# Kernel optimization log

Hardware: AMD Instinct MI355X
Metric: run time of the kernel (lower is better)

Reference implementation:

```python
import jax, jax.numpy as jnp
import numpy as np

EMBED_DIM = 512
NUM_HEADS = 8
HEAD_DIM = EMBED_DIM // NUM_HEADS
N_NODES = 65536
EPS = 1e-5


def setup_inputs() -> dict:
    key = jax.random.key(0)
    ks = jax.random.split(key, 16)
    std = 0.02
    E, F = EMBED_DIM, 4 * EMBED_DIM
    return {
        "x": jax.random.normal(ks[0], (N_NODES, E), jnp.float32),
        "Wq": jax.random.normal(ks[1], (E, E), jnp.float32) * std,
        "bq": jnp.zeros((E,), jnp.float32),
        "Wk": jax.random.normal(ks[2], (E, E), jnp.float32) * std,
        "bk": jnp.zeros((E,), jnp.float32),
        "Wv": jax.random.normal(ks[3], (E, E), jnp.float32) * std,
        "bv": jnp.zeros((E,), jnp.float32),
        "Wo": jax.random.normal(ks[4], (E, E), jnp.float32) * std,
        "bo": jnp.zeros((E,), jnp.float32),
        "W1": jax.random.normal(ks[5], (F, E), jnp.float32) * std,
        "b1": jnp.zeros((F,), jnp.float32),
        "W2": jax.random.normal(ks[6], (E, F), jnp.float32) * std,
        "b2": jnp.zeros((E,), jnp.float32),
        "g1": jnp.ones((E,), jnp.float32),
        "beta1": jnp.zeros((E,), jnp.float32),
        "g2": jnp.ones((E,), jnp.float32),
        "beta2": jnp.zeros((E,), jnp.float32),
    }


def _layernorm(x, g, b):
    mu = jnp.mean(x, axis=-1, keepdims=True)
    var = jnp.mean(jnp.square(x - mu), axis=-1, keepdims=True)
    return (x - mu) * jax.lax.rsqrt(var + EPS) * g + b


def reference(x, Wq, bq, Wk, bk, Wv, bv, Wo, bo, W1, b1, W2, b2, g1, beta1, g2, beta2):
    N = x.shape[0]
    H, D = NUM_HEADS, HEAD_DIM
    residual = x
    h = _layernorm(x, g1, beta1)
    q = (h @ Wq.T + bq).reshape(N, H, D)
    k = (h @ Wk.T + bk).reshape(N, H, D)
    v = (h @ Wv.T + bv).reshape(N, H, D)
    # per-node attention across heads: scores (N, H, H)
    scores = jnp.einsum('nhd,ngd->nhg', q, k) / np.float32(np.sqrt(D))
    attn = jax.nn.softmax(scores, axis=-1)
    out = jnp.einsum('nhg,ngd->nhd', attn, v).reshape(N, H * D)
    out = out @ Wo.T + bo
    x = residual + out  # dropout is identity in eval
    residual = x
    h = _layernorm(x, g2, beta2)
    ff = jax.nn.relu(h @ W1.T + b1) @ W2.T + b2
    return residual + ff
```

## Files before the change

kernel.cpp:

```cpp
#include <hip/hip_runtime.h>
#include <hip/hip_bf16.h>
#include <stdint.h>

typedef __hip_bfloat16 bf16;
typedef short bf16x8 __attribute__((ext_vector_type(8)));
typedef float f32x4 __attribute__((ext_vector_type(4)));

typedef __attribute__((address_space(1))) const unsigned int as1_uint;
typedef __attribute__((address_space(3))) unsigned int as3_uint;

__device__ __forceinline__ void async_copy16(const void* g, void* l) {
    __builtin_amdgcn_global_load_lds((as1_uint*)g, (as3_uint*)l, 16, 0, 0);
}

__device__ __forceinline__ float b2f(unsigned short u) {
    union { unsigned int i; float f; } c; c.i = ((unsigned int)u) << 16; return c.f;
}
__device__ __forceinline__ unsigned short f2b(float f) {
    union { float f; unsigned int i; } c; c.f = f;
    unsigned int i = c.i;
    i += 0x7fffu + ((i >> 16) & 1u);
    return (unsigned short)(i >> 16);
}

__global__ __launch_bounds__(256)
void cvt_kernel(const float* __restrict__ in, bf16* __restrict__ out)
{
    const int i = (blockIdx.x * 256 + threadIdx.x) * 8;
    const float4 a = *(const float4*)(in + i);
    const float4 b = *(const float4*)(in + i + 4);
    union { uint4 v; unsigned short s[8]; } u;
    u.s[0] = f2b(a.x); u.s[1] = f2b(a.y); u.s[2] = f2b(a.z); u.s[3] = f2b(a.w);
    u.s[4] = f2b(b.x); u.s[5] = f2b(b.y); u.s[6] = f2b(b.z); u.s[7] = f2b(b.w);
    *(uint4*)((unsigned short*)out + i) = u.v;
}

__global__ __launch_bounds__(256)
void ln_kernel(const float* __restrict__ x, const float* __restrict__ g,
               const float* __restrict__ beta, bf16* __restrict__ out)
{
    const int w = threadIdx.x >> 6, l = threadIdx.x & 63;
    const int n = blockIdx.x * 4 + w;

    const float* xr = x + (size_t)n * 512 + l * 8;
    const float4 a = *(const float4*)xr;
    const float4 b = *(const float4*)(xr + 4);
    float f[8] = {a.x, a.y, a.z, a.w, b.x, b.y, b.z, b.w};

    float s = 0.f, q = 0.f;
#pragma unroll
    for (int i = 0; i < 8; ++i) { s += f[i]; q += f[i] * f[i]; }
#pragma unroll
    for (int o = 32; o > 0; o >>= 1) { s += __shfl_xor(s, o); q += __shfl_xor(q, o); }
    const float mean = s * (1.f / 512.f);
    const float var  = q * (1.f / 512.f) - mean * mean;
    const float rstd = rsqrtf(var + 1e-5f);

    const float4 g0 = *(const float4*)(g + l * 8);
    const float4 g1 = *(const float4*)(g + l * 8 + 4);
    const float4 b0 = *(const float4*)(beta + l * 8);
    const float4 b1 = *(const float4*)(beta + l * 8 + 4);
    const float gg[8] = {g0.x,g0.y,g0.z,g0.w,g1.x,g1.y,g1.z,g1.w};
    const float bb[8] = {b0.x,b0.y,b0.z,b0.w,b1.x,b1.y,b1.z,b1.w};

    union { uint4 v; unsigned short s[8]; } o;
#pragma unroll
    for (int i = 0; i < 8; ++i)
        o.s[i] = f2b((f[i] - mean) * rstd * gg[i] + bb[i]);
    *(uint4*)((unsigned short*)out + (size_t)n * 512 + l * 8) = o.v;
}

__global__ __launch_bounds__(256)
void attn_kernel(const bf16* __restrict__ qkv, bf16* __restrict__ out)
{
    __shared__ unsigned short sm[4][1536];
    const int w = threadIdx.x >> 6, l = threadIdx.x & 63;
    const int n = blockIdx.x * 4 + w;

    const uint4* src = (const uint4*)((const unsigned short*)qkv + (size_t)n * 1536);
    uint4* dst = (uint4*)sm[w];
#pragma unroll
    for (int i = 0; i < 3; ++i) dst[i * 64 + l] = src[i * 64 + l];
    __syncthreads();

    const int h = l >> 3, gi = l & 7;
    const unsigned short* qrow = sm[w] + h * 64;
    const unsigned short* krow = sm[w] + 512 + gi * 64;
    float s = 0.f;
#pragma unroll
    for (int jj = 0; jj < 8; ++jj) {
        union { uint4 v; unsigned short s8[8]; } qa, ka;
        qa.v = *(const uint4*)(qrow + jj * 8);
        ka.v = *(const uint4*)(krow + jj * 8);
#pragma unroll
        for (int j = 0; j < 8; ++j) s += b2f(qa.s8[j]) * b2f(ka.s8[j]);
    }
    s *= 0.125f;

    float m = s;
#pragma unroll
    for (int o = 1; o < 8; o <<= 1) m = fmaxf(m, __shfl_xor(m, o));
    float e = __expf(s - m);
    float d = e;
#pragma unroll
    for (int o = 1; o < 8; o <<= 1) d += __shfl_xor(d, o);
    const float p = e / d;

    float acc[8];
#pragma unroll
    for (int j = 0; j < 8; ++j) acc[j] = 0.f;
    const int j8 = (l & 7) * 8;
#pragma unroll
    for (int gg = 0; gg < 8; ++gg) {
        const float pg = __shfl(p, (l & 56) | gg);
        union { uint4 v; unsigned short s8[8]; } va;
        va.v = *(const uint4*)(sm[w] + 1024 + gg * 64 + j8);
#pragma unroll
        for (int j = 0; j < 8; ++j) acc[j] += pg * b2f(va.s8[j]);
    }
    union { uint4 v; unsigned short s8[8]; } o;
#pragma unroll
    for (int j = 0; j < 8; ++j) o.s8[j] = f2b(acc[j]);
    *(uint4*)((unsigned short*)out + (size_t)n * 512 + h * 64 + j8) = o.v;
}

#define EPI_PLAIN 0
#define EPI_RES   1
#define EPI_RELU  2

template<int MODE>
__global__ __launch_bounds__(512, 2)
void gemm_bt(const bf16* __restrict__ A,
             const bf16* __restrict__ B0, const bf16* __restrict__ B1,
             const bf16* __restrict__ B2,
             const float* __restrict__ bias0, const float* __restrict__ bias1,
             const float* __restrict__ bias2,
             const float* __restrict__ res,
             void* __restrict__ C,
             int K, int Nper, int ldc)
{
    __shared__ bf16 As[2][2][8192];
    __shared__ bf16 Bs[2][2][8192];

    const int tid = threadIdx.x;
    const int w = tid >> 6, l = tid & 63;

    const int nbx = gridDim.x;
    const int nwg = nbx * (int)gridDim.y;
    int lid = blockIdx.y * nbx + blockIdx.x;
    {
        const int q = nwg >> 3, r = nwg & 7;
        const int xcd = lid & 7, idx = lid >> 3;
        lid = (xcd < r ? xcd * (q + 1) : r * (q + 1) + (xcd - r) * q) + idx;
    }
    const int bx = lid % nbx, by = lid / nbx;

    const int rowBase = by * 256;
    const int colBase = bx * 256;
    const int sel = colBase / Nper;
    const bf16*  B    = (sel == 0) ? B0 : (sel == 1) ? B1 : B2;
    const float* bias = (sel == 0) ? bias0 : (sel == 1) ? bias1 : bias2;
    const int colInB = colBase - sel * Nper;

    const bf16* Ag = A + (size_t)rowBase * K;
    const bf16* Bg = B + (size_t)colInB * K;

    const int wr = w >> 2, wc = w & 3;
    const int ml = l & 15;
    const int kc = l >> 4;
    const int rdoff = ((kc ^ ((ml >> 1) & 3)) << 3);

    const int s_row = l >> 2;
    const int s_koff = (((l & 3) ^ ((l >> 3) & 3)) << 3);

    auto stA = [&](int t, int half) {
#pragma unroll
        for (int c = 0; c < 2; ++c) {
            const int q = (w << 1) | c;
            const int p = q >> 3, rr = q & 7;
            const bf16* src = Ag + (size_t)(half * 128 + rr * 16 + s_row) * K
                            + (t << 6) + p * 32 + s_koff;
            async_copy16(src, &As[t & 1][half][q << 9]);
        }
    };
    auto stB = [&](int t, int half) {
#pragma unroll
        for (int c = 0; c < 2; ++c) {
            const int q = (w << 1) | c;
            const int p = q >> 3, rr = q & 7;
            const bf16* src = Bg + (size_t)(half * 128 + rr * 16 + s_row) * K
                            + (t << 6) + p * 32 + s_koff;
            async_copy16(src, &Bs[t & 1][half][q << 9]);
        }
    };

    const int bRow = ((wc & 1) << 6) + ml;
    const int bHalf = wc >> 1;

    f32x4 acc[8][4];
#pragma unroll
    for (int i = 0; i < 8; ++i)
#pragma unroll
        for (int j = 0; j < 4; ++j) acc[i][j] = (f32x4)(0.f);

    bf16x8 af[4][2], bf[4][2];

#define LDA(SLOT, MI, KS) \
    (*(const bf16x8*)(&As[SLOT][wr][(KS) * 4096 + ((MI) * 16 + ml) * 32 + rdoff]))
#define LDB(SLOT, NI, KS) \
    (*(const bf16x8*)(&Bs[SLOT][bHalf][(KS) * 4096 + (bRow + (NI) * 16) * 32 + rdoff]))

#define MMQ(MG, NG) \
    do { \
        _Pragma("unroll") \
        for (int mi = 0; mi < 4; ++mi) \
        _Pragma("unroll") \
        for (int nj = 0; nj < 2; ++nj) \
        _Pragma("unroll") \
        for (int ks = 0; ks < 2; ++ks) \
            acc[(MG)*4+mi][(NG)*2+nj] = __builtin_amdgcn_mfma_f32_16x16x32_bf16( \
                af[mi][ks], bf[(NG)*2+nj][ks], acc[(MG)*4+mi][(NG)*2+nj], 0, 0, 0); \
    } while (0)

#define SYNC_IN()  do { __builtin_amdgcn_s_barrier(); \
                        __builtin_amdgcn_sched_barrier(0); \
                        asm volatile("s_waitcnt lgkmcnt(0)" ::: "memory"); \
                        __builtin_amdgcn_sched_barrier(0); } while (0)
#define SYNC_OUT() do { __builtin_amdgcn_s_barrier(); \
                        __builtin_amdgcn_sched_barrier(0); } while (0)

    const int NT = K >> 6;
    const int NI = NT >> 1;

    stA(0, 0); stA(0, 1); stB(0, 0); stB(0, 1);
    stA(1, 0); stB(1, 0);
    asm volatile("s_waitcnt vmcnt(4)" ::: "memory");
    __builtin_amdgcn_s_barrier();
    __builtin_amdgcn_sched_barrier(0);

    for (int i = 0; i < NI; ++i) {
        const int t1 = 2 * i + 1;
        const bool pf = (t1 + 1 < NT);

#pragma unroll
        for (int mi = 0; mi < 4; ++mi) { af[mi][0] = LDA(0, mi, 0); af[mi][1] = LDA(0, mi, 1); }
#pragma unroll
        for (int nj = 0; nj < 2; ++nj) { bf[nj][0] = LDB(0, nj, 0); bf[nj][1] = LDB(0, nj, 1); }
        stA(t1, 1);
        SYNC_IN();
        __builtin_amdgcn_s_setprio(1); MMQ(0, 0); __builtin_amdgcn_s_setprio(0);
        SYNC_OUT();

#pragma unroll
        for (int nj = 2; nj < 4; ++nj) { bf[nj][0] = LDB(0, nj, 0); bf[nj][1] = LDB(0, nj, 1); }
        stB(t1, 1);
        SYNC_IN();
        __builtin_amdgcn_s_setprio(1); MMQ(0, 1); __builtin_amdgcn_s_setprio(0);
        SYNC_OUT();

#pragma unroll
        for (int mi = 0; mi < 4; ++mi) { af[mi][0] = LDA(0, mi + 4, 0); af[mi][1] = LDA(0, mi + 4, 1); }
        if (pf) stB(t1 + 1, 0);
        SYNC_IN();
        __builtin_amdgcn_s_setprio(1); MMQ(1, 0); __builtin_amdgcn_s_setprio(0);
        SYNC_OUT();

        if (pf) stB(t1 + 1, 1);
        __builtin_amdgcn_s_barrier();
        __builtin_amdgcn_sched_barrier(0);
        __builtin_amdgcn_s_setprio(1); MMQ(1, 1); __builtin_amdgcn_s_setprio(0);
        if (pf) asm volatile("s_waitcnt vmcnt(4)" ::: "memory");
        else    asm volatile("s_waitcnt vmcnt(0)" ::: "memory");
        SYNC_OUT();

#pragma unroll
        for (int mi = 0; mi < 4; ++mi) { af[mi][0] = LDA(1, mi, 0); af[mi][1] = LDA(1, mi, 1); }
#pragma unroll
        for (int nj = 0; nj < 2; ++nj) { bf[nj][0] = LDB(1, nj, 0); bf[nj][1] = LDB(1, nj, 1); }
        if (pf) stA(t1 + 1, 0);
        SYNC_IN();
        __builtin_amdgcn_s_setprio(1); MMQ(0, 0); __builtin_amdgcn_s_setprio(0);
        SYNC_OUT();

#pragma unroll
        for (int nj = 2; nj < 4; ++nj) { bf[nj][0] = LDB(1, nj, 0); bf[nj][1] = LDB(1, nj, 1); }
        if (pf) stA(t1 + 1, 1);
        SYNC_IN();
        __builtin_amdgcn_s_setprio(1); MMQ(0, 1); __builtin_amdgcn_s_setprio(0);
        SYNC_OUT();

#pragma unroll
        for (int mi = 0; mi < 4; ++mi) { af[mi][0] = LDA(1, mi + 4, 0); af[mi][1] = LDA(1, mi + 4, 1); }
        if (pf) stB(t1 + 2, 0);
        SYNC_IN();
        __builtin_amdgcn_s_setprio(1); MMQ(1, 0); __builtin_amdgcn_s_setprio(0);
        SYNC_OUT();

        if (pf) stA(t1 + 2, 0);
        __builtin_amdgcn_s_barrier();
        __builtin_amdgcn_sched_barrier(0);
        __builtin_amdgcn_s_setprio(1); MMQ(1, 1); __builtin_amdgcn_s_setprio(0);
        if (pf) asm volatile("s_waitcnt vmcnt(4)" ::: "memory");
        if (i < NI - 1) SYNC_OUT();
    }

    float bv[4];
#pragma unroll
    for (int ni = 0; ni < 4; ++ni)
        bv[ni] = bias[colInB + (wc << 6) + (ni << 4) + ml];

#pragma unroll
    for (int mi = 0; mi < 8; ++mi) {
#pragma unroll
        for (int r4 = 0; r4 < 4; ++r4) {
            const int row = rowBase + (wr << 7) + (mi << 4) + (kc << 2) + r4;
            const size_t rowoff = (size_t)row * ldc;
#pragma unroll
            for (int ni = 0; ni < 4; ++ni) {
                const int gcol = colBase + (wc << 6) + (ni << 4) + ml;
                float v = acc[mi][ni][r4] + bv[ni];
                if (MODE == EPI_RELU) v = fmaxf(v, 0.f);
                if (MODE == EPI_RES) {
                    v += res[rowoff + gcol];
                    ((float*)C)[rowoff + gcol] = v;
                } else {
                    ((unsigned short*)C)[rowoff + gcol] = f2b(v);
                }
            }
        }
    }
#undef LDA
#undef LDB
#undef MMQ
#undef SYNC_IN
#undef SYNC_OUT
}

extern "C" void kernel_launch(void* const* d_in, const int* in_sizes, int n_in,
                              void* d_out, int out_size, void* d_ws, size_t ws_size,
                              hipStream_t stream)
{
    const float* x   = (const float*)d_in[0];
    const float* Wq  = (const float*)d_in[1];
    const float* bq  = (const float*)d_in[2];
    const float* Wk  = (const float*)d_in[3];
    const float* bk  = (const float*)d_in[4];
    const float* Wv  = (const float*)d_in[5];
    const float* bv  = (const float*)d_in[6];
    const float* Wo  = (const float*)d_in[7];
    const float* bo  = (const float*)d_in[8];
    const float* W1  = (const float*)d_in[9];
    const float* b1  = (const float*)d_in[10];
    const float* W2  = (const float*)d_in[11];
    const float* b2  = (const float*)d_in[12];
    const float* g1  = (const float*)d_in[13];
    const float* be1 = (const float*)d_in[14];
    const float* g2  = (const float*)d_in[15];
    const float* be2 = (const float*)d_in[16];

    const int N = 65536;

    bf16* Wqb = (bf16*)d_ws;
    bf16* Wkb = Wqb + 262144;
    bf16* Wvb = Wkb + 262144;
    bf16* Wob = Wvb + 262144;
    bf16* W1b = Wob + 262144;
    bf16* W2b = W1b + 1048576;
    const size_t wts_bytes = 6ull * 1024 * 1024;
    bf16* t64 = (bf16*)((char*)d_ws + wts_bytes);
    const size_t t64_bytes = (size_t)N * 512 * 2;
    bf16* cb  = (bf16*)((char*)d_ws + wts_bytes + t64_bytes);
    const size_t used = wts_bytes + t64_bytes;
    const size_t avail = ws_size > used ? ws_size - used : 0;
    int Nc = 32768;
    while (Nc > 256 && (size_t)Nc * 4096 > avail) Nc >>= 1;

    float* x2 = (float*)d_out;
    dim3 blk(256);
    dim3 blk5(512);

    cvt_kernel<<<262144 / 2048, blk, 0, stream>>>(Wq, Wqb);
    cvt_kernel<<<262144 / 2048, blk, 0, stream>>>(Wk, Wkb);
    cvt_kernel<<<262144 / 2048, blk, 0, stream>>>(Wv, Wvb);
    cvt_kernel<<<262144 / 2048, blk, 0, stream>>>(Wo, Wob);
    cvt_kernel<<<1048576 / 2048, blk, 0, stream>>>(W1, W1b);
    cvt_kernel<<<1048576 / 2048, blk, 0, stream>>>(W2, W2b);

    ln_kernel<<<N / 4, blk, 0, stream>>>(x, g1, be1, t64);

    for (int r0 = 0; r0 < N; r0 += Nc) {
        gemm_bt<EPI_PLAIN><<<dim3(6, Nc / 256), blk5, 0, stream>>>(
            t64 + (size_t)r0 * 512, Wqb, Wkb, Wvb, bq, bk, bv, nullptr,
            cb, 512, 512, 1536);
        attn_kernel<<<Nc / 4, blk, 0, stream>>>(cb, t64 + (size_t)r0 * 512);
    }

    gemm_bt<EPI_RES><<<dim3(2, N / 256), blk5, 0, stream>>>(
        t64, Wob, Wob, Wob, bo, bo, bo, x, x2, 512, 512, 512);

    ln_kernel<<<N / 4, blk, 0, stream>>>(x2, g2, be2, t64);

    for (int r0 = 0; r0 < N; r0 += Nc) {
        gemm_bt<EPI_RELU><<<dim3(8, Nc / 256), blk5, 0, stream>>>(
            t64 + (size_t)r0 * 512, W1b, W1b, W1b, b1, b1, b1, nullptr,
            cb, 512, 2048, 2048);
        gemm_bt<EPI_RES><<<dim3(2, Nc / 256), blk5, 0, stream>>>(
            cb, W2b, W2b, W2b, b2, b2, b2, x2 + (size_t)r0 * 512,
            x2 + (size_t)r0 * 512, 2048, 512, 512);
    }
}
```

Before: 925.5 us.

## Fuse FFN up-projection, ReLU, and down-projection into one kernel

Replaces the two chunked FFN GEMMs with a single kernel that keeps a 64-node tile of the normalized activations in LDS. It computes 256-wide slices of the hidden layer with ReLU into double-buffered LDS and accumulates the W2 product in registers, so the large bf16 hidden tensor never goes to global memory. Weights are read straight from global memory with no LDS staging, and each block handles only 64 nodes with a single block per CU, which may cost weight bandwidth and latency hiding. The load order in the existing GEMM prologue is also interleaved, and the chunk-size workspace check is adjusted.

New measurement: 1.128 ms. +21.9%, slower.

```diff
diff --git a/kernel.cpp b/kernel.cpp
--- a/kernel.cpp
+++ b/kernel.cpp
@@ -232,7 +232,7 @@
     const int NT = K >> 6;
     const int NI = NT >> 1;
 
-    stA(0, 0); stA(0, 1); stB(0, 0); stB(0, 1);
+    stA(0, 0); stB(0, 0); stA(0, 1); stB(0, 1);
     stA(1, 0); stB(1, 0);
     asm volatile("s_waitcnt vmcnt(4)" ::: "memory");
     __builtin_amdgcn_s_barrier();
@@ -334,6 +334,139 @@
 #undef MMQ
 #undef SYNC_IN
 #undef SYNC_OUT
+}
+
+__global__ __launch_bounds__(512, 1)
+void ffn_fused(const bf16* __restrict__ h2,
+               const bf16* __restrict__ W1,
+               const bf16* __restrict__ W2,
+               const float* __restrict__ b1,
+               const float* __restrict__ b2,
+               float* __restrict__ xio)
+{
+    __shared__ bf16 hs[16 * 64 * 32];
+    __shared__ bf16 ps[2 * 64 * 256];
+
+    const int tid = threadIdx.x;
+    const int w = tid >> 6, l = tid & 63;
+    const int node0 = blockIdx.x * 64;
+    const int ml = l & 15, lh = l >> 4;
+
+    {
+        const int sr = l >> 2;
+        const int sk = (((l & 3) ^ ((sr >> 1) & 3)) << 3);
+#pragma unroll
+        for (int j = 0; j < 8; ++j) {
+            const int q = j * 8 + w;
+            const int pl = q >> 2, rg = q & 3;
+            const bf16* src = h2 + (size_t)(node0 + rg * 16 + sr) * 512
+                            + pl * 32 + sk;
+            async_copy16(src, &hs[q << 9]);
+        }
+    }
+    asm volatile("s_waitcnt vmcnt(0)" ::: "memory");
+    __syncthreads();
+
+    const int rdk = ((lh ^ ((ml >> 1) & 3)) << 3);
+
+    f32x4 acc2[4][4];
+#pragma unroll
+    for (int i = 0; i < 4; ++i)
+#pragma unroll
+        for (int j = 0; j < 4; ++j) acc2[i][j] = (f32x4)(0.f);
+
+    for (int s = 0; s < 8; ++s) {
+        f32x4 pacc[2][4];
+#pragma unroll
+        for (int i = 0; i < 2; ++i)
+#pragma unroll
+            for (int j = 0; j < 4; ++j) pacc[i][j] = (f32x4)(0.f);
+
+        const bf16* w1base = W1 + (size_t)(s * 256 + w * 32) * 512;
+#pragma unroll
+        for (int kt = 0; kt < 8; ++kt) {
+            bf16x8 afp[2][2], bfp[4][2];
+#pragma unroll
+            for (int mi = 0; mi < 2; ++mi)
+#pragma unroll
+                for (int ks = 0; ks < 2; ++ks)
+                    afp[mi][ks] = *(const bf16x8*)(w1base
+                        + (size_t)(mi * 16 + ml) * 512 + kt * 64 + ks * 32 + lh * 8);
+#pragma unroll
+            for (int ni = 0; ni < 4; ++ni)
+#pragma unroll
+                for (int ks = 0; ks < 2; ++ks)
+                    bfp[ni][ks] = *(const bf16x8*)(&hs[(kt * 2 + ks) * 2048
+                        + (ni * 16 + ml) * 32 + rdk]);
+#pragma unroll
+            for (int mi = 0; mi < 2; ++mi)
+#pragma unroll
+                for (int ni = 0; ni < 4; ++ni)
+#pragma unroll
+                    for (int ks = 0; ks < 2; ++ks)
+                        pacc[mi][ni] = __builtin_amdgcn_mfma_f32_16x16x32_bf16(
+                            afp[mi][ks], bfp[ni][ks], pacc[mi][ni], 0, 0, 0);
+        }
+
+        const int buf = (s & 1) << 14;
+#pragma unroll
+        for (int mi = 0; mi < 2; ++mi) {
+            const float4 bb = *(const float4*)(b1 + s * 256 + w * 32 + mi * 16 + lh * 4);
+            const float b4[4] = {bb.x, bb.y, bb.z, bb.w};
+#pragma unroll
+            for (int ni = 0; ni < 4; ++ni) {
+                const int row = ni * 16 + ml;
+                const int col = (w * 32 + mi * 16 + lh * 4) ^ ((row & 7) << 3);
+                union { uint2 v; unsigned short s4[4]; } o;
+#pragma unroll
+                for (int r = 0; r < 4; ++r)
+                    o.s4[r] = f2b(fmaxf(pacc[mi][ni][r] + b4[r], 0.f));
+                *(uint2*)(&ps[buf + row * 256 + col]) = o.v;
+            }
+        }
+        __syncthreads();
+
+        const bf16* w2base = W2 + (size_t)(w * 64) * 2048 + s * 256;
+#pragma unroll
+        for (int kt2 = 0; kt2 < 8; ++kt2) {
+            bf16x8 af2[4], bf2[4];
+#pragma unroll
+            for (int of = 0; of < 4; ++of)
+                af2[of] = *(const bf16x8*)(w2base
+                    + (size_t)(of * 16 + ml) * 2048 + kt2 * 32 + lh * 8);
+#pragma unroll
+            for (int nf = 0; nf < 4; ++nf) {
+                const int row = nf * 16 + ml;
+                const int col = (kt2 * 32 + lh * 8) ^ ((row & 7) << 3);
+                bf2[nf] = *(const bf16x8*)(&ps[buf + row * 256 + col]);
+            }
+#pragma unroll
+            for (int of = 0; of < 4; ++of)
+#pragma unroll
+                for (int nf = 0; nf < 4; ++nf)
+                    acc2[of][nf] = __builtin_amdgcn_mfma_f32_16x16x32_bf16(
+                        af2[of], bf2[nf], acc2[of][nf], 0, 0, 0);
+        }
+        __syncthreads();
+    }
+
+#pragma unroll
+    for (int of = 0; of < 4; ++of) {
+        const int oc0 = w * 64 + of * 16 + lh * 4;
+        const float4 bb = *(const float4*)(b2 + oc0);
+#pragma unroll
+        for (int nf = 0; nf < 4; ++nf) {
+            const int node = node0 + nf * 16 + ml;
+            float4* p = (float4*)(xio + (size_t)node * 512 + oc0);
+            const float4 r = *p;
+            float4 o;
+            o.x = acc2[of][nf][0] + r.x + bb.x;
+            o.y = acc2[of][nf][1] + r.y + bb.y;
+            o.z = acc2[of][nf][2] + r.z + bb.z;
+            o.w = acc2[of][nf][3] + r.w + bb.w;
+            *p = o;
+        }
+    }
 }
 
 extern "C" void kernel_launch(void* const* d_in, const int* in_sizes, int n_in,
@@ -373,7 +506,7 @@
     const size_t used = wts_bytes + t64_bytes;
     const size_t avail = ws_size > used ? ws_size - used : 0;
     int Nc = 32768;
-    while (Nc > 256 && (size_t)Nc * 4096 > avail) Nc >>= 1;
+    while (Nc > 256 && (size_t)Nc * 3072 > avail) Nc >>= 1;
 
     float* x2 = (float*)d_out;
     dim3 blk(256);
@@ -400,12 +533,5 @@
 
     ln_kernel<<<N / 4, blk, 0, stream>>>(x2, g2, be2, t64);
 
-    for (int r0 = 0; r0 < N; r0 += Nc) {
-        gemm_bt<EPI_RELU><<<dim3(8, Nc / 256), blk5, 0, stream>>>(
-            t64 + (size_t)r0 * 512, W1b, W1b, W1b, b1, b1, b1, nullptr,
-            cb, 512, 2048, 2048);
-        gemm_bt<EPI_RES><<<dim3(2, Nc / 256), blk5, 0, stream>>>(
-            cb, W2b, W2b, W2b, b2, b2, b2, x2 + (size_t)r0 * 512,
-            x2 + (size_t)r0 * 512, 2048, 512, 512);
-    }
-}
+    ffn_fused<<<N / 64, blk5, 0, stream>>>(t64, W1b, W2b, b1, b2, x2);
+}
```
